# Optimization experiments

Hardware: AMD Instinct MI355X
Metric: run time of the kernel (lower is better)

The kernel has to match this reference:

```python
import jax, jax.numpy as jnp
import numpy as np

B = 16        # batch
V = 49152     # HEALPix nside=64 vertices
CIN = 32
COUT = 64
K = 4         # Chebyshev polynomial degree (kernel_size)
NNZ = V * 9   # ~9 nonzeros per row of the sparse Laplacian
POOL = 4      # HEALPix pooling factor
EPS = 1e-5    # BatchNorm eps


def setup_inputs() -> dict:
    key = jax.random.key(0)
    k1, k2, k3, k4, k5 = jax.random.split(key, 5)
    x = jax.random.normal(k1, (B, V, CIN), dtype=jnp.float32)
    lap_rows = jnp.sort(jax.random.randint(k2, (NNZ,), 0, V, dtype=jnp.int32)).astype(jnp.int64)
    lap_cols = jax.random.randint(k3, (NNZ,), 0, V, dtype=jnp.int32).astype(jnp.int64)
    lap_vals = jax.random.normal(k4, (NNZ,), dtype=jnp.float32) * 0.1
    weight = jax.random.normal(k5, (K, CIN, COUT), dtype=jnp.float32) / np.sqrt(K * CIN).astype(np.float32)
    gamma = jnp.ones((COUT,), dtype=jnp.float32)
    beta = jnp.zeros((COUT,), dtype=jnp.float32)
    return {"x": x, "lap_vals": lap_vals, "weight": weight, "gamma": gamma,
            "beta": beta, "lap_rows": lap_rows, "lap_cols": lap_cols}


def _spmm(rows, cols, vals, X):
    """Sparse [V,V] @ dense [V,F] via gather + segment_sum."""
    return jax.ops.segment_sum(vals[:, None] * X[cols], rows, num_segments=V)


def reference(x, lap_vals, weight, gamma, beta, lap_rows, lap_cols):
    b, v, c = x.shape
    # Chebyshev recurrence on [V, B*Cin] layout (vertex-major for spmm)
    X0 = x.transpose(1, 0, 2).reshape(v, b * c)
    xs = [X0]
    X1 = _spmm(lap_rows, lap_cols, lap_vals, X0)
    xs.append(X1)
    for _ in range(K - 2):
        X2 = 2.0 * _spmm(lap_rows, lap_cols, lap_vals, X1) - X0
        xs.append(X2)
        X0, X1 = X1, X2
    cheb = jnp.stack(xs, axis=0).reshape(K, v, b, c)   # [K,V,B,Cin]
    y = jnp.einsum('kvbi,kio->bvo', cheb, weight)      # [B,V,Cout]
    # BatchNorm1d(Cout), training-mode stats over (batch, vertices), biased var
    mean = jnp.mean(y, axis=(0, 1))
    var = jnp.var(y, axis=(0, 1))
    y = (y - mean) * jax.lax.rsqrt(var + EPS) * gamma + beta
    y = jax.nn.relu(y)
    # HEALPix average pooling (factor 4) over vertex dim
    out = y.reshape(b, v // POOL, POOL, COUT).mean(axis=2)
    return out
```

## Files before the change

kernel.cpp:

```cpp
#include <hip/hip_runtime.h>
#include <hip/hip_bf16.h>

#define V     49152
#define NNZ   442368
#define EPS   1e-5f
#define VOUT  12288

typedef __attribute__((ext_vector_type(8))) short bf16x8;
typedef __attribute__((ext_vector_type(4))) float f32x4;

__device__ __forceinline__ unsigned short f2b(float f) {
    __hip_bfloat16 h = __float2bfloat16(f);
    return *reinterpret_cast<unsigned short*>(&h);
}
__device__ __forceinline__ float b2f(unsigned short u) {
    return __uint_as_float((unsigned)u << 16);
}

__global__ __launch_bounds__(256) void k_rowptr(const int* __restrict__ rows,
                                                int* __restrict__ rp) {
    int id = blockIdx.x * blockDim.x + threadIdx.x;
    if (id <= V) {
        int lo = 0, hi = NNZ;
        while (lo < hi) {
            int m = (lo + hi) >> 1;
            if (rows[m] < id) lo = m + 1; else hi = m;
        }
        rp[id] = lo;
    }
}

__global__ __launch_bounds__(256) void k_xpose(const float* __restrict__ x,
                                               unsigned short* __restrict__ xbf) {
    int id = blockIdx.x * 256 + threadIdx.x;
    int i4 = id & 7;
    int b  = (id >> 3) & 15;
    int v  = id >> 7;
    float4 q = *(const float4*)&x[((size_t)b * V + v) * 32 + i4 * 4];
    ushort4 u = {f2b(q.x), f2b(q.y), f2b(q.z), f2b(q.w)};
    *(ushort4*)&xbf[(size_t)v * 512 + b * 32 + i4 * 4] = u;
}

__global__ __launch_bounds__(256) void k_wconv(const float* __restrict__ W,
                                               unsigned short* __restrict__ Wfrag) {
    int d = blockIdx.x * 256 + threadIdx.x;
    int j = d & 7, lane = (d >> 3) & 63, ct = (d >> 9) & 3, ks = d >> 11;
    int k128 = ks * 32 + (lane >> 4) * 8 + j;
    int o = ct * 16 + (lane & 15);
    Wfrag[d] = f2b(W[k128 * 64 + o]);
}

#define GATHER_LOOP(SRC)                                                        \
    float a[8] = {0.f, 0.f, 0.f, 0.f, 0.f, 0.f, 0.f, 0.f};                      \
    int n = s;                                                                  \
    for (; n + 3 < e; n += 4) {                                                 \
        int c0 = cols[n], c1 = cols[n + 1], c2 = cols[n + 2], c3 = cols[n + 3]; \
        float w0 = vals[n], w1 = vals[n + 1], w2 = vals[n + 2], w3 = vals[n + 3]; \
        union { unsigned short u[8]; uint4 q; } l0, l1, l2, l3;                 \
        l0.q = *(const uint4*)&SRC[(size_t)c0 * 512 + f0];                      \
        l1.q = *(const uint4*)&SRC[(size_t)c1 * 512 + f0];                      \
        l2.q = *(const uint4*)&SRC[(size_t)c2 * 512 + f0];                      \
        l3.q = *(const uint4*)&SRC[(size_t)c3 * 512 + f0];                      \
        _Pragma("unroll")                                                       \
        for (int j = 0; j < 8; ++j) a[j] = fmaf(w0, b2f(l0.u[j]), a[j]);        \
        _Pragma("unroll")                                                       \
        for (int j = 0; j < 8; ++j) a[j] = fmaf(w1, b2f(l1.u[j]), a[j]);        \
        _Pragma("unroll")                                                       \
        for (int j = 0; j < 8; ++j) a[j] = fmaf(w2, b2f(l2.u[j]), a[j]);        \
        _Pragma("unroll")                                                       \
        for (int j = 0; j < 8; ++j) a[j] = fmaf(w3, b2f(l3.u[j]), a[j]);        \
    }                                                                           \
    for (; n < e; ++n) {                                                        \
        int c0 = cols[n];                                                       \
        float w0 = vals[n];                                                     \
        union { unsigned short u[8]; uint4 q; } l0;                             \
        l0.q = *(const uint4*)&SRC[(size_t)c0 * 512 + f0];                      \
        _Pragma("unroll")                                                       \
        for (int j = 0; j < 8; ++j) a[j] = fmaf(w0, b2f(l0.u[j]), a[j]);        \
    }

__global__ __launch_bounds__(256) void k_spmm1(const unsigned short* __restrict__ xbf,
                                               const int* __restrict__ cols,
                                               const float* __restrict__ vals,
                                               const int* __restrict__ rp,
                                               unsigned short* __restrict__ X1) {
    int t = threadIdx.x;
    int wave = t >> 6, lane = t & 63;
    int v = blockIdx.x * 4 + wave;
    int f0 = lane * 8;
    int s = rp[v], e = rp[v + 1];
    GATHER_LOOP(xbf)
    union { unsigned short u[8]; uint4 q; } st;
#pragma unroll
    for (int j = 0; j < 8; ++j) st.u[j] = f2b(a[j]);
    *(uint4*)&X1[(size_t)v * 512 + f0] = st.q;
}

__global__ __launch_bounds__(256) void k_spmm2(const unsigned short* __restrict__ xbf,
                                               const int* __restrict__ cols,
                                               const float* __restrict__ vals,
                                               const int* __restrict__ rp,
                                               const unsigned short* __restrict__ X1,
                                               unsigned short* __restrict__ X2) {
    int t = threadIdx.x;
    int wave = t >> 6, lane = t & 63;
    int v = blockIdx.x * 4 + wave;
    int f0 = lane * 8;
    int s = rp[v], e = rp[v + 1];
    GATHER_LOOP(X1)
    union { unsigned short u[8]; uint4 q; } x0;
    x0.q = *(const uint4*)&xbf[(size_t)v * 512 + f0];
    union { unsigned short u[8]; uint4 q; } st;
#pragma unroll
    for (int j = 0; j < 8; ++j) st.u[j] = f2b(2.f * a[j] - b2f(x0.u[j]));
    *(uint4*)&X2[(size_t)v * 512 + f0] = st.q;
}

__global__ __launch_bounds__(256) void k_spmm3(const unsigned short* __restrict__ X1,
                                               const int* __restrict__ cols,
                                               const float* __restrict__ vals,
                                               const int* __restrict__ rp,
                                               const unsigned short* __restrict__ X2,
                                               unsigned short* __restrict__ X3) {
    int t = threadIdx.x;
    int wave = t >> 6, lane = t & 63;
    int v = blockIdx.x * 4 + wave;
    int f0 = lane * 8;
    int s = rp[v], e = rp[v + 1];
    GATHER_LOOP(X2)
    union { unsigned short u[8]; uint4 q; } p1;
    p1.q = *(const uint4*)&X1[(size_t)v * 512 + f0];
    union { unsigned short u[8]; uint4 q; } st;
#pragma unroll
    for (int j = 0; j < 8; ++j) st.u[j] = f2b(2.f * a[j] - b2f(p1.u[j]));
    *(uint4*)&X3[(size_t)v * 512 + f0] = st.q;
}

__global__ __launch_bounds__(256) void k_einsum(const unsigned short* __restrict__ xbf,
                                                const unsigned short* __restrict__ X1,
                                                const unsigned short* __restrict__ X2,
                                                const unsigned short* __restrict__ X3,
                                                const unsigned short* __restrict__ Wfrag,
                                                unsigned short* __restrict__ Y,
                                                float* __restrict__ pout) {
    __shared__ unsigned short sB[8192];
    __shared__ unsigned short sY[4096];
    __shared__ float sP[512];

    int t = threadIdx.x;
    int wave = t >> 6, lane = t & 63;
    int v = blockIdx.x * 4 + wave;

#pragma unroll
    for (int m = 0; m < 4; ++m) {
        int d = t + m * 256;
        *(uint4*)&sB[d * 8] = *(const uint4*)&Wfrag[d * 8];
    }
    __syncthreads();

    f32x4 acc[4];
#pragma unroll
    for (int ct = 0; ct < 4; ++ct) acc[ct] = (f32x4){0.f, 0.f, 0.f, 0.f};

    const unsigned short* srcs[4] = {xbf, X1, X2, X3};
    size_t abase = (size_t)v * 512 + (lane & 15) * 32 + (lane >> 4) * 8;
#pragma unroll
    for (int ks = 0; ks < 4; ++ks) {
        bf16x8 a = *(const bf16x8*)&srcs[ks][abase];
#pragma unroll
        for (int ct = 0; ct < 4; ++ct) {
            bf16x8 b = *(const bf16x8*)&sB[((ks * 4 + ct) * 64 + lane) * 8];
            acc[ct] = __builtin_amdgcn_mfma_f32_16x16x32_bf16(a, b, acc[ct], 0, 0, 0);
        }
    }

#pragma unroll
    for (int ct = 0; ct < 4; ++ct) {
        float ss = acc[ct].x + acc[ct].y + acc[ct].z + acc[ct].w;
        float qq = acc[ct].x * acc[ct].x + acc[ct].y * acc[ct].y
                 + acc[ct].z * acc[ct].z + acc[ct].w * acc[ct].w;
        ss += __shfl_xor(ss, 16); ss += __shfl_xor(ss, 32);
        qq += __shfl_xor(qq, 16); qq += __shfl_xor(qq, 32);
        if (lane < 16) {
            sP[wave * 128 + ct * 16 + lane]      = ss;
            sP[wave * 128 + 64 + ct * 16 + lane] = qq;
        }
    }

#pragma unroll
    for (int ct = 0; ct < 4; ++ct) {
        int o = ct * 16 + (lane & 15);
        int bb = (lane >> 4) * 4;
        sY[wave * 1024 + (bb + 0) * 64 + o] = f2b(acc[ct].x);
        sY[wave * 1024 + (bb + 1) * 64 + o] = f2b(acc[ct].y);
        sY[wave * 1024 + (bb + 2) * 64 + o] = f2b(acc[ct].z);
        sY[wave * 1024 + (bb + 3) * 64 + o] = f2b(acc[ct].w);
    }
    __syncthreads();

    size_t ybase = (size_t)blockIdx.x * 4096 + t * 16;
    *(uint4*)&Y[ybase]     = *(const uint4*)&sY[t * 16];
    *(uint4*)&Y[ybase + 8] = *(const uint4*)&sY[t * 16 + 8];

    if (t < 128)
        pout[(size_t)blockIdx.x * 1024 + t] =
            sP[t] + sP[128 + t] + sP[256 + t] + sP[384 + t];
}

__global__ __launch_bounds__(128) void k_bnred2(const float* __restrict__ P,
                                                float* __restrict__ partials2) {
    int t = threadIdx.x;
    size_t base = (size_t)blockIdx.x * 256;
    float s = 0.f;
    for (int r = 0; r < 256; ++r)
        s += P[(base + r) * 1024 + t];
    partials2[blockIdx.x * 128 + t] = s;
}

__global__ void k_bnfin(const float* __restrict__ partials2,
                        const float* __restrict__ gamma, const float* __restrict__ beta,
                        float* __restrict__ stats) {
    __shared__ float tot[128];
    int t = threadIdx.x;
    float s = 0.f;
    for (int i = 0; i < 48; ++i) s += partials2[i * 128 + t];
    tot[t] = s;
    __syncthreads();
    if (t < 64) {
        float n = (float)(16 * V);
        float mean = tot[t] / n;
        float var = tot[64 + t] / n - mean * mean;
        float sc = gamma[t] * rsqrtf(var + EPS);
        stats[128 + t] = sc;
        stats[192 + t] = beta[t] - mean * sc;
    }
}

__global__ __launch_bounds__(256) void k_pool(const unsigned short* __restrict__ Y,
                                              const float* __restrict__ stats,
                                              float* __restrict__ out) {
    int id = blockIdx.x * blockDim.x + threadIdx.x;
    int o4 = id & 15;
    int b  = (id >> 4) & 15;
    int vp = id >> 8;
    float4 sc = *(const float4*)&stats[128 + o4 * 4];
    float4 sh = *(const float4*)&stats[192 + o4 * 4];
    float ax = 0.f, ay = 0.f, az = 0.f, aw = 0.f;
#pragma unroll
    for (int j = 0; j < 4; ++j) {
        ushort4 u = *(const ushort4*)&Y[(size_t)((vp * 4 + j) * 16 + b) * 64 + o4 * 4];
        float tx = b2f(u.x), ty = b2f(u.y), tz = b2f(u.z), tw = b2f(u.w);
        ax += fmaxf(fmaf(tx, sc.x, sh.x), 0.f);
        ay += fmaxf(fmaf(ty, sc.y, sh.y), 0.f);
        az += fmaxf(fmaf(tz, sc.z, sh.z), 0.f);
        aw += fmaxf(fmaf(tw, sc.w, sh.w), 0.f);
    }
    float4 res = {ax * 0.25f, ay * 0.25f, az * 0.25f, aw * 0.25f};
    *(float4*)&out[(size_t)((b * VOUT + vp) * 16 + o4) * 4] = res;
}

extern "C" void kernel_launch(void* const* d_in, const int* in_sizes, int n_in,
                              void* d_out, int out_size, void* d_ws, size_t ws_size,
                              hipStream_t stream) {
    const float* x     = (const float*)d_in[0];
    const float* vals  = (const float*)d_in[1];
    const float* W     = (const float*)d_in[2];
    const float* gamma = (const float*)d_in[3];
    const float* beta  = (const float*)d_in[4];
    const int*   rows  = (const int*)d_in[5];
    const int*   cols  = (const int*)d_in[6];
    float* out = (float*)d_out;

    char* ws = (char*)d_ws;
    unsigned short* xbf = (unsigned short*)ws;
    unsigned short* X1  = (unsigned short*)(ws + 50331648UL);
    unsigned short* X2  = (unsigned short*)(ws + 100663296UL);
    unsigned short* X3  = (unsigned short*)(ws + 150994944UL);
    unsigned short* Y   = (unsigned short*)(ws + 201326592UL);
    int*   rp    = (int*)(ws + 301989888UL);
    float* stats = (float*)(ws + 302186560UL);
    unsigned short* Wfrag = (unsigned short*)(ws + 302187584UL);
    float* partials2 = (float*)(ws + 302204032UL);

    k_rowptr<<<193, 256, 0, stream>>>(rows, rp);
    k_xpose<<<V * 128 / 256, 256, 0, stream>>>(x, xbf);
    k_wconv<<<32, 256, 0, stream>>>(W, Wfrag);
    k_spmm1<<<V / 4, 256, 0, stream>>>(xbf, cols, vals, rp, X1);
    k_spmm2<<<V / 4, 256, 0, stream>>>(xbf, cols, vals, rp, X1, X2);
    k_spmm3<<<V / 4, 256, 0, stream>>>(X1, cols, vals, rp, X2, X3);
    k_einsum<<<V / 4, 256, 0, stream>>>(xbf, X1, X2, X3, Wfrag, Y, (float*)X3);
    k_bnred2<<<48, 128, 0, stream>>>((const float*)X3, partials2);
    k_bnfin<<<1, 128, 0, stream>>>(partials2, gamma, beta, stats);
    k_pool<<<12288, 256, 0, stream>>>(Y, stats, out);
}
```

Before: 353.9 us.

## Fuse third Chebyshev SpMM into the MFMA einsum kernel via lane shuffles

```diff
diff --git a/kernel.cpp b/kernel.cpp
--- a/kernel.cpp
+++ b/kernel.cpp
@@ -116,62 +116,66 @@
     *(uint4*)&X2[(size_t)v * 512 + f0] = st.q;
 }
 
-__global__ __launch_bounds__(256) void k_spmm3(const unsigned short* __restrict__ X1,
-                                               const int* __restrict__ cols,
-                                               const float* __restrict__ vals,
-                                               const int* __restrict__ rp,
-                                               const unsigned short* __restrict__ X2,
-                                               unsigned short* __restrict__ X3) {
+__global__ __launch_bounds__(256) void k_cheb(const unsigned short* __restrict__ xbf,
+                                              const unsigned short* __restrict__ X1,
+                                              const unsigned short* __restrict__ X2,
+                                              const unsigned short* __restrict__ Wfrag,
+                                              const int* __restrict__ cols,
+                                              const float* __restrict__ vals,
+                                              const int* __restrict__ rp,
+                                              unsigned short* __restrict__ Y,
+                                              float* __restrict__ pout) {
+    __shared__ unsigned short sB[8192];
+    __shared__ unsigned short sY[4096];
+
     int t = threadIdx.x;
     int wave = t >> 6, lane = t & 63;
     int v = blockIdx.x * 4 + wave;
+
+#pragma unroll
+    for (int m = 0; m < 4; ++m) {
+        int d = t + m * 256;
+        *(uint4*)&sB[d * 8] = *(const uint4*)&Wfrag[d * 8];
+    }
+
     int f0 = lane * 8;
     int s = rp[v], e = rp[v + 1];
     GATHER_LOOP(X2)
     union { unsigned short u[8]; uint4 q; } p1;
     p1.q = *(const uint4*)&X1[(size_t)v * 512 + f0];
-    union { unsigned short u[8]; uint4 q; } st;
-#pragma unroll
-    for (int j = 0; j < 8; ++j) st.u[j] = f2b(2.f * a[j] - b2f(p1.u[j]));
-    *(uint4*)&X3[(size_t)v * 512 + f0] = st.q;
-}
-
-__global__ __launch_bounds__(256) void k_einsum(const unsigned short* __restrict__ xbf,
-                                                const unsigned short* __restrict__ X1,
-                                                const unsigned short* __restrict__ X2,
-                                                const unsigned short* __restrict__ X3,
-                                                const unsigned short* __restrict__ Wfrag,
-                                                unsigned short* __restrict__ Y,
-                                                float* __restrict__ pout) {
-    __shared__ unsigned short sB[8192];
-    __shared__ unsigned short sY[4096];
-    __shared__ float sP[512];
-
-    int t = threadIdx.x;
-    int wave = t >> 6, lane = t & 63;
-    int v = blockIdx.x * 4 + wave;
-
-#pragma unroll
-    for (int m = 0; m < 4; ++m) {
-        int d = t + m * 256;
-        *(uint4*)&sB[d * 8] = *(const uint4*)&Wfrag[d * 8];
-    }
+    uint4 packed;
+    packed.x = (unsigned)f2b(2.f * a[0] - b2f(p1.u[0])) | ((unsigned)f2b(2.f * a[1] - b2f(p1.u[1])) << 16);
+    packed.y = (unsigned)f2b(2.f * a[2] - b2f(p1.u[2])) | ((unsigned)f2b(2.f * a[3] - b2f(p1.u[3])) << 16);
+    packed.z = (unsigned)f2b(2.f * a[4] - b2f(p1.u[4])) | ((unsigned)f2b(2.f * a[5] - b2f(p1.u[5])) << 16);
+    packed.w = (unsigned)f2b(2.f * a[6] - b2f(p1.u[6])) | ((unsigned)f2b(2.f * a[7] - b2f(p1.u[7])) << 16);
+    int src = (lane & 15) * 4 + (lane >> 4);
+    union { uint4 q; bf16x8 h; } a3;
+    a3.q.x = __shfl(packed.x, src);
+    a3.q.y = __shfl(packed.y, src);
+    a3.q.z = __shfl(packed.z, src);
+    a3.q.w = __shfl(packed.w, src);
+
     __syncthreads();
 
     f32x4 acc[4];
 #pragma unroll
     for (int ct = 0; ct < 4; ++ct) acc[ct] = (f32x4){0.f, 0.f, 0.f, 0.f};
 
-    const unsigned short* srcs[4] = {xbf, X1, X2, X3};
+    const unsigned short* srcs[3] = {xbf, X1, X2};
     size_t abase = (size_t)v * 512 + (lane & 15) * 32 + (lane >> 4) * 8;
 #pragma unroll
-    for (int ks = 0; ks < 4; ++ks) {
-        bf16x8 a = *(const bf16x8*)&srcs[ks][abase];
+    for (int ks = 0; ks < 3; ++ks) {
+        bf16x8 af = *(const bf16x8*)&srcs[ks][abase];
 #pragma unroll
         for (int ct = 0; ct < 4; ++ct) {
             bf16x8 b = *(const bf16x8*)&sB[((ks * 4 + ct) * 64 + lane) * 8];
-            acc[ct] = __builtin_amdgcn_mfma_f32_16x16x32_bf16(a, b, acc[ct], 0, 0, 0);
+            acc[ct] = __builtin_amdgcn_mfma_f32_16x16x32_bf16(af, b, acc[ct], 0, 0, 0);
         }
+    }
+#pragma unroll
+    for (int ct = 0; ct < 4; ++ct) {
+        bf16x8 b = *(const bf16x8*)&sB[((12 + ct) * 64 + lane) * 8];
+        acc[ct] = __builtin_amdgcn_mfma_f32_16x16x32_bf16(a3.h, b, acc[ct], 0, 0, 0);
     }
 
 #pragma unroll
@@ -182,8 +186,9 @@
         ss += __shfl_xor(ss, 16); ss += __shfl_xor(ss, 32);
         qq += __shfl_xor(qq, 16); qq += __shfl_xor(qq, 32);
         if (lane < 16) {
-            sP[wave * 128 + ct * 16 + lane]      = ss;
-            sP[wave * 128 + 64 + ct * 16 + lane] = qq;
+            float* pw = &pout[(size_t)(blockIdx.x * 4 + wave) * 128];
+            pw[ct * 16 + lane]      = ss;
+            pw[64 + ct * 16 + lane] = qq;
         }
     }
 
@@ -197,23 +202,18 @@
         sY[wave * 1024 + (bb + 3) * 64 + o] = f2b(acc[ct].w);
     }
     __syncthreads();
-
     size_t ybase = (size_t)blockIdx.x * 4096 + t * 16;
     *(uint4*)&Y[ybase]     = *(const uint4*)&sY[t * 16];
     *(uint4*)&Y[ybase + 8] = *(const uint4*)&sY[t * 16 + 8];
-
-    if (t < 128)
-        pout[(size_t)blockIdx.x * 1024 + t] =
-            sP[t] + sP[128 + t] + sP[256 + t] + sP[384 + t];
 }
 
 __global__ __launch_bounds__(128) void k_bnred2(const float* __restrict__ P,
                                                 float* __restrict__ partials2) {
     int t = threadIdx.x;
-    size_t base = (size_t)blockIdx.x * 256;
+    size_t base = (size_t)blockIdx.x * 1024;
     float s = 0.f;
-    for (int r = 0; r < 256; ++r)
-        s += P[(base + r) * 1024 + t];
+    for (int r = 0; r < 1024; ++r)
+        s += P[(base + r) * 128 + t];
     partials2[blockIdx.x * 128 + t] = s;
 }
 
@@ -275,21 +275,20 @@
     unsigned short* xbf = (unsigned short*)ws;
     unsigned short* X1  = (unsigned short*)(ws + 50331648UL);
     unsigned short* X2  = (unsigned short*)(ws + 100663296UL);
-    unsigned short* X3  = (unsigned short*)(ws + 150994944UL);
-    unsigned short* Y   = (unsigned short*)(ws + 201326592UL);
-    int*   rp    = (int*)(ws + 301989888UL);
-    float* stats = (float*)(ws + 302186560UL);
-    unsigned short* Wfrag = (unsigned short*)(ws + 302187584UL);
-    float* partials2 = (float*)(ws + 302204032UL);
+    unsigned short* Y   = (unsigned short*)(ws + 150994944UL);
+    int*   rp    = (int*)(ws + 251658240UL);
+    float* stats = (float*)(ws + 251859968UL);
+    unsigned short* Wfrag = (unsigned short*)(ws + 251860992UL);
+    float* pout  = (float*)(ws + 251877376UL);
+    float* partials2 = (float*)(ws + 277043200UL);
 
     k_rowptr<<<193, 256, 0, stream>>>(rows, rp);
     k_xpose<<<V * 128 / 256, 256, 0, stream>>>(x, xbf);
     k_wconv<<<32, 256, 0, stream>>>(W, Wfrag);
     k_spmm1<<<V / 4, 256, 0, stream>>>(xbf, cols, vals, rp, X1);
     k_spmm2<<<V / 4, 256, 0, stream>>>(xbf, cols, vals, rp, X1, X2);
-    k_spmm3<<<V / 4, 256, 0, stream>>>(X1, cols, vals, rp, X2, X3);
-    k_einsum<<<V / 4, 256, 0, stream>>>(xbf, X1, X2, X3, Wfrag, Y, (float*)X3);
-    k_bnred2<<<48, 128, 0, stream>>>((const float*)X3, partials2);
+    k_cheb<<<V / 4, 256, 0, stream>>>(xbf, X1, X2, Wfrag, cols, vals, rp, Y, pout);
+    k_bnred2<<<48, 128, 0, stream>>>(pout, partials2);
     k_bnfin<<<1, 128, 0, stream>>>(partials2, gamma, beta, stats);
     k_pool<<<12288, 256, 0, stream>>>(Y, stats, out);
 }
```

After: 351.0 us. About the same (-0.8%).
